# Performance work log

Measured on AMD Instinct MI355X. Metric: run time of the kernel, lower is better.

The kernel has to match this reference:

```python
import jax, jax.numpy as jnp
import numpy as np

N = 10000
D_IN = 128
HID = 32
EMB = 16


def setup_inputs() -> dict:
    key = jax.random.key(0)
    k0, k1, k2, k3 = jax.random.split(key, 4)
    X = jax.random.normal(k0, (N, D_IN), dtype=jnp.float32)
    # nonnegative, row-stochastic-ish prior
    A = jax.random.uniform(k1, (N, N), dtype=jnp.float32, minval=1e-6, maxval=1.0)
    A_prior = A / jnp.sum(A, axis=1, keepdims=True)
    # kaiming_uniform(a=sqrt(5)) on torch Linear weight (fan_in = D_IN): bound = 1/sqrt(fan_in)
    bnd1 = 1.0 / np.sqrt(D_IN)
    W1 = jax.random.uniform(k2, (D_IN, HID), dtype=jnp.float32, minval=-bnd1, maxval=bnd1)
    b1 = jnp.zeros((HID,), dtype=jnp.float32)
    # xavier_uniform: bound = sqrt(6/(fan_in+fan_out))
    bnd2 = np.sqrt(6.0 / (HID + EMB))
    W2 = jax.random.uniform(k3, (HID, EMB), dtype=jnp.float32, minval=-bnd2, maxval=bnd2)
    b2 = jnp.zeros((EMB,), dtype=jnp.float32)
    log_tau = jnp.asarray(np.log(1.2), dtype=jnp.float32)
    raw_alpha = jnp.asarray(np.log(0.3 / 0.7), dtype=jnp.float32)
    return {"X": X, "A_prior": A_prior, "W1": W1, "b1": b1, "W2": W2, "b2": b2,
            "log_tau": log_tau, "raw_alpha": raw_alpha}


def reference(X, A_prior, W1, b1, W2, b2, log_tau, raw_alpha):
    # encoder: Linear -> ReLU -> Linear
    H = jax.nn.relu(X @ W1 + b1) @ W2 + b2            # (N, EMB)
    # F.normalize(p=2, dim=1): x / max(||x||, eps)
    Hn = H / jnp.maximum(jnp.linalg.norm(H, axis=1, keepdims=True), 1e-12)
    tau = jnp.clip(jnp.exp(log_tau), 0.1, 10.0)
    alpha = jax.nn.sigmoid(raw_alpha)
    logits = (Hn @ Hn.T) / tau                        # (N, N) cosine sims / tau
    log_combined = alpha * jnp.log(A_prior + 1e-12) + (1.0 - alpha) * logits
    W = jax.nn.softmax(log_combined, axis=1)          # row-stochastic (N, N)
    return (W, H)
```

## Files before the change

kernel.cpp:

```cpp
#include <hip/hip_runtime.h>
#include <math.h>

#define N_NODES 10000
#define DIN 128
#define HID 32
#define EMB 16

#define TBS 256
#define RB 4
#define NF4 2500
#define NIT ((NF4 + TBS - 1) / TBS)
#define NB (N_NODES / RB)

typedef float fx4 __attribute__((ext_vector_type(4)));

#define EXP2F(x) __builtin_amdgcn_exp2f(x)
#define LOG2F(x) __builtin_amdgcn_logf(x)

__global__ __launch_bounds__(256) void encoder_kernel(
    const float* __restrict__ X, const float* __restrict__ W1,
    const float* __restrict__ b1, const float* __restrict__ W2,
    const float* __restrict__ b2, float* __restrict__ Hout,
    float* __restrict__ Hn)
{
    __shared__ float sW1[DIN * HID];
    __shared__ float sW2[HID * EMB];
    __shared__ float sb1[HID];
    __shared__ float sb2[EMB];
    const int t = threadIdx.x;
    for (int k = t; k < DIN * HID; k += 256) sW1[k] = W1[k];
    for (int k = t; k < HID * EMB; k += 256) sW2[k] = W2[k];
    if (t < HID) sb1[t] = b1[t];
    if (t < EMB) sb2[t] = b2[t];
    __syncthreads();

    const int row = blockIdx.x * 256 + t;
    if (row >= N_NODES) return;

    float h1[HID];
#pragma unroll
    for (int h = 0; h < HID; ++h) h1[h] = sb1[h];

    const float4* xr = (const float4*)(X + (size_t)row * DIN);
#pragma unroll
    for (int k4 = 0; k4 < DIN / 4; ++k4) {
        float4 xv = xr[k4];
        const float* w = &sW1[(k4 * 4) * HID];
#pragma unroll
        for (int h = 0; h < HID; ++h) h1[h] = fmaf(xv.x, w[h], h1[h]);
#pragma unroll
        for (int h = 0; h < HID; ++h) h1[h] = fmaf(xv.y, w[HID + h], h1[h]);
#pragma unroll
        for (int h = 0; h < HID; ++h) h1[h] = fmaf(xv.z, w[2 * HID + h], h1[h]);
#pragma unroll
        for (int h = 0; h < HID; ++h) h1[h] = fmaf(xv.w, w[3 * HID + h], h1[h]);
    }

    float e[EMB];
#pragma unroll
    for (int j = 0; j < EMB; ++j) e[j] = sb2[j];
#pragma unroll
    for (int h = 0; h < HID; ++h) {
        float v = fmaxf(h1[h], 0.0f);
#pragma unroll
        for (int j = 0; j < EMB; ++j) e[j] = fmaf(v, sW2[h * EMB + j], e[j]);
    }

    float s = 0.0f;
#pragma unroll
    for (int j = 0; j < EMB; ++j) s = fmaf(e[j], e[j], s);
    float nrm = sqrtf(s);
    float inv = 1.0f / fmaxf(nrm, 1e-12f);

    float* ho = Hout + (size_t)row * EMB;
    float* hn = Hn + (size_t)row * EMB;
#pragma unroll
    for (int j = 0; j < EMB; ++j) ho[j] = e[j];
#pragma unroll
    for (int j = 0; j < EMB; ++j) hn[j] = e[j] * inv;
}


__device__ __forceinline__ float dot16u(const float* h, const fx4& b0,
                                        const fx4& b1, const fx4& b2,
                                        const fx4& b3)
{
    float s = h[0] * b0.x;
    s = fmaf(h[1],  b0.y, s);
    s = fmaf(h[2],  b0.z, s);
    s = fmaf(h[3],  b0.w, s);
    s = fmaf(h[4],  b1.x, s);
    s = fmaf(h[5],  b1.y, s);
    s = fmaf(h[6],  b1.z, s);
    s = fmaf(h[7],  b1.w, s);
    s = fmaf(h[8],  b2.x, s);
    s = fmaf(h[9],  b2.y, s);
    s = fmaf(h[10], b2.z, s);
    s = fmaf(h[11], b2.w, s);
    s = fmaf(h[12], b3.x, s);
    s = fmaf(h[13], b3.y, s);
    s = fmaf(h[14], b3.z, s);
    s = fmaf(h[15], b3.w, s);
    return s;
}

__global__ __launch_bounds__(TBS, 8) void softmax_kernel(
    const float* __restrict__ A, const float* __restrict__ Hn,
    const float* __restrict__ p_log_tau, const float* __restrict__ p_raw_alpha,
    float* __restrict__ Wout)
{
    const int t = threadIdx.x;
    const int row0 = blockIdx.x * RB;

    const float tau = fminf(fmaxf(__expf(p_log_tau[0]), 0.1f), 10.0f);
    const float alpha = 1.0f / (1.0f + __expf(-p_raw_alpha[0]));
    const float cl  = (1.0f - alpha) / tau;
    const float cl2 = cl * 1.4426950408889634f;

    float shi[RB][EMB];
#pragma unroll
    for (int r = 0; r < RB; ++r) {
        const fx4* hp = (const fx4*)(Hn + (size_t)(row0 + r) * EMB);
#pragma unroll
        for (int p = 0; p < 4; ++p) {
            fx4 v = hp[p];
            shi[r][4 * p + 0] = __int_as_float(__builtin_amdgcn_readfirstlane(__float_as_int(v.x)));
            shi[r][4 * p + 1] = __int_as_float(__builtin_amdgcn_readfirstlane(__float_as_int(v.y)));
            shi[r][4 * p + 2] = __int_as_float(__builtin_amdgcn_readfirstlane(__float_as_int(v.z)));
            shi[r][4 * p + 3] = __int_as_float(__builtin_amdgcn_readfirstlane(__float_as_int(v.w)));
        }
    }

    const fx4* Hn4 = (const fx4*)Hn;

    float sloc[RB];
#pragma unroll
    for (int r = 0; r < RB; ++r) sloc[r] = 0.0f;

#pragma unroll 2
    for (int it = 0; it < NIT; ++it) {
        const int f4 = it * TBS + t;
        if (f4 < NF4) {
            fx4 av[RB];
#pragma unroll
            for (int r = 0; r < RB; ++r)
                av[r] = *((const fx4*)(A + (size_t)(row0 + r) * N_NODES) + f4);
#pragma unroll
            for (int d = 0; d < 4; ++d) {
                const int j = f4 * 4 + d;
                const fx4 b0 = Hn4[j * 4 + 0];
                const fx4 b1 = Hn4[j * 4 + 1];
                const fx4 b2 = Hn4[j * 4 + 2];
                const fx4 b3 = Hn4[j * 4 + 3];
#pragma unroll
                for (int r = 0; r < RB; ++r) {
                    float a = (d == 0) ? av[r].x
                            : (d == 1) ? av[r].y
                            : (d == 2) ? av[r].z
                                       : av[r].w;
                    float lgm = fmaf(alpha, LOG2F(a + 1e-12f), -cl2);
                    float dv = dot16u(shi[r], b0, b1, b2, b3);
                    sloc[r] += EXP2F(fmaf(cl2, dv, lgm));
                }
            }
        }
    }

    __shared__ float red[RB][TBS / 64];
    __shared__ float rbc[RB];
    const int lane = t & 63;
    const int wave = t >> 6;
#pragma unroll
    for (int r = 0; r < RB; ++r) {
        float v = sloc[r];
#pragma unroll
        for (int off = 32; off >= 1; off >>= 1) v += __shfl_down(v, off, 64);
        if (lane == 0) red[r][wave] = v;
    }
    __syncthreads();
    if (t < RB) {
        float v = red[t][0];
#pragma unroll
        for (int w = 1; w < TBS / 64; ++w) v += red[t][w];
        rbc[t] = 1.0f / v;
    }
    __syncthreads();
    float invl[RB];
#pragma unroll
    for (int r = 0; r < RB; ++r) invl[r] = rbc[r];

#pragma unroll 2
    for (int it = NIT - 1; it >= 0; --it) {
        const int f4 = it * TBS + t;
        if (f4 < NF4) {
            fx4 av[RB];
#pragma unroll
            for (int r = 0; r < RB; ++r)
                av[r] = __builtin_nontemporal_load(
                    (const fx4*)(A + (size_t)(row0 + r) * N_NODES) + f4);
            fx4 o[RB];
#pragma unroll
            for (int d = 0; d < 4; ++d) {
                const int j = f4 * 4 + d;
                const fx4 b0 = Hn4[j * 4 + 0];
                const fx4 b1 = Hn4[j * 4 + 1];
                const fx4 b2 = Hn4[j * 4 + 2];
                const fx4 b3 = Hn4[j * 4 + 3];
#pragma unroll
                for (int r = 0; r < RB; ++r) {
                    float a = (d == 0) ? av[r].x
                            : (d == 1) ? av[r].y
                            : (d == 2) ? av[r].z
                                       : av[r].w;
                    float lgm = fmaf(alpha, LOG2F(a + 1e-12f), -cl2);
                    float dv = dot16u(shi[r], b0, b1, b2, b3);
                    float e = EXP2F(fmaf(cl2, dv, lgm)) * invl[r];
                    if (d == 0)      o[r].x = e;
                    else if (d == 1) o[r].y = e;
                    else if (d == 2) o[r].z = e;
                    else             o[r].w = e;
                }
            }
#pragma unroll
            for (int r = 0; r < RB; ++r)
                __builtin_nontemporal_store(
                    o[r], (fx4*)(Wout + (size_t)(row0 + r) * N_NODES) + f4);
        }
    }
}

extern "C" void kernel_launch(void* const* d_in, const int* in_sizes, int n_in,
                              void* d_out, int out_size, void* d_ws, size_t ws_size,
                              hipStream_t stream) {
    const float* X        = (const float*)d_in[0];
    const float* A        = (const float*)d_in[1];
    const float* W1       = (const float*)d_in[2];
    const float* b1       = (const float*)d_in[3];
    const float* W2       = (const float*)d_in[4];
    const float* b2       = (const float*)d_in[5];
    const float* log_tau  = (const float*)d_in[6];
    const float* raw_alpha= (const float*)d_in[7];

    float* Wout = (float*)d_out;
    float* Hout = (float*)d_out + (size_t)N_NODES * N_NODES;
    float* Hn   = (float*)d_ws;

    encoder_kernel<<<(N_NODES + 255) / 256, 256, 0, stream>>>(X, W1, b1, W2, b2, Hout, Hn);

    softmax_kernel<<<NB, TBS, 0, stream>>>(A, Hn, log_tau, raw_alpha, Wout);
}
```

Measured before the change: 1.219 ms.

## Split softmax into 2D-tiled partial-sum and normalize kernels with LDS transposed tiles

Replaces the single row-block softmax kernel with two kernels over a 2D grid of (256-row block, 200-column group). Each thread now owns one row and keeps its Hn vector in registers. A and W tiles are staged through LDS so global accesses stay coalesced while each thread works along its own row. Per-group partial sums go to workspace and the second kernel sums all 50 partials before normalizing. This trades the old per-block wide row reduction and the reload of Hn for each row block for an extra launch, additional workspace traffic, strided LDS access, and Hn column loads that are uniform across a wave (broadcast).

```diff
diff --git a/kernel.cpp b/kernel.cpp
--- a/kernel.cpp
+++ b/kernel.cpp
@@ -6,11 +6,13 @@
 #define HID 32
 #define EMB 16
 
-#define TBS 256
-#define RB 4
-#define NF4 2500
-#define NIT ((NF4 + TBS - 1) / TBS)
-#define NB (N_NODES / RB)
+#define RBLK 256
+#define G    50
+#define JG   200
+#define JT   20
+#define NTILE (JG / JT)
+#define LSTR 24
+#define NRB  ((N_NODES + RBLK - 1) / RBLK)
 
 typedef float fx4 __attribute__((ext_vector_type(4)));
 
@@ -81,150 +83,157 @@
 }
 
 
-__device__ __forceinline__ float dot16u(const float* h, const fx4& b0,
-                                        const fx4& b1, const fx4& b2,
-                                        const fx4& b3)
-{
-    float s = h[0] * b0.x;
-    s = fmaf(h[1],  b0.y, s);
-    s = fmaf(h[2],  b0.z, s);
-    s = fmaf(h[3],  b0.w, s);
-    s = fmaf(h[4],  b1.x, s);
-    s = fmaf(h[5],  b1.y, s);
-    s = fmaf(h[6],  b1.z, s);
-    s = fmaf(h[7],  b1.w, s);
-    s = fmaf(h[8],  b2.x, s);
-    s = fmaf(h[9],  b2.y, s);
-    s = fmaf(h[10], b2.z, s);
-    s = fmaf(h[11], b2.w, s);
-    s = fmaf(h[12], b3.x, s);
-    s = fmaf(h[13], b3.y, s);
-    s = fmaf(h[14], b3.z, s);
-    s = fmaf(h[15], b3.w, s);
+__device__ __forceinline__ float dot16f(const float4& ha, const float4& hb,
+                                        const float4& hc, const float4& hd,
+                                        const float4& b0, const float4& b1,
+                                        const float4& b2, const float4& b3)
+{
+    float s = ha.x * b0.x;
+    s = fmaf(ha.y, b0.y, s);
+    s = fmaf(ha.z, b0.z, s);
+    s = fmaf(ha.w, b0.w, s);
+    s = fmaf(hb.x, b1.x, s);
+    s = fmaf(hb.y, b1.y, s);
+    s = fmaf(hb.z, b1.z, s);
+    s = fmaf(hb.w, b1.w, s);
+    s = fmaf(hc.x, b2.x, s);
+    s = fmaf(hc.y, b2.y, s);
+    s = fmaf(hc.z, b2.z, s);
+    s = fmaf(hc.w, b2.w, s);
+    s = fmaf(hd.x, b3.x, s);
+    s = fmaf(hd.y, b3.y, s);
+    s = fmaf(hd.z, b3.z, s);
+    s = fmaf(hd.w, b3.w, s);
     return s;
 }
 
-__global__ __launch_bounds__(TBS, 8) void softmax_kernel(
+__global__ __launch_bounds__(RBLK, 6) void partial_kernel(
     const float* __restrict__ A, const float* __restrict__ Hn,
     const float* __restrict__ p_log_tau, const float* __restrict__ p_raw_alpha,
-    float* __restrict__ Wout)
-{
+    float* __restrict__ partial)
+{
+    __shared__ float lds[RBLK * LSTR];
     const int t = threadIdx.x;
-    const int row0 = blockIdx.x * RB;
+    const int row0 = blockIdx.x * RBLK;
+    const int g = blockIdx.y;
+    const int j0 = g * JG;
 
     const float tau = fminf(fmaxf(__expf(p_log_tau[0]), 0.1f), 10.0f);
     const float alpha = 1.0f / (1.0f + __expf(-p_raw_alpha[0]));
-    const float cl  = (1.0f - alpha) / tau;
-    const float cl2 = cl * 1.4426950408889634f;
-
-    float shi[RB][EMB];
-#pragma unroll
-    for (int r = 0; r < RB; ++r) {
-        const fx4* hp = (const fx4*)(Hn + (size_t)(row0 + r) * EMB);
-#pragma unroll
-        for (int p = 0; p < 4; ++p) {
-            fx4 v = hp[p];
-            shi[r][4 * p + 0] = __int_as_float(__builtin_amdgcn_readfirstlane(__float_as_int(v.x)));
-            shi[r][4 * p + 1] = __int_as_float(__builtin_amdgcn_readfirstlane(__float_as_int(v.y)));
-            shi[r][4 * p + 2] = __int_as_float(__builtin_amdgcn_readfirstlane(__float_as_int(v.z)));
-            shi[r][4 * p + 3] = __int_as_float(__builtin_amdgcn_readfirstlane(__float_as_int(v.w)));
-        }
-    }
-
-    const fx4* Hn4 = (const fx4*)Hn;
-
-    float sloc[RB];
-#pragma unroll
-    for (int r = 0; r < RB; ++r) sloc[r] = 0.0f;
-
-#pragma unroll 2
-    for (int it = 0; it < NIT; ++it) {
-        const int f4 = it * TBS + t;
-        if (f4 < NF4) {
-            fx4 av[RB];
-#pragma unroll
-            for (int r = 0; r < RB; ++r)
-                av[r] = *((const fx4*)(A + (size_t)(row0 + r) * N_NODES) + f4);
+    const float cl2 = ((1.0f - alpha) / tau) * 1.4426950408889634f;
+
+    const int rowc = min(row0 + t, N_NODES - 1);
+    const float4* hp = (const float4*)(Hn + (size_t)rowc * EMB);
+    const float4 ha = hp[0], hb = hp[1], hc = hp[2], hd = hp[3];
+
+    float sloc = 0.0f;
+
+    for (int tile = 0; tile < NTILE; ++tile) {
+        const int jt0 = j0 + tile * JT;
+        __syncthreads();
+#pragma unroll
+        for (int k = 0; k < 5; ++k) {
+            const int f = k * RBLK + t;
+            const int r = f / 5, q = f % 5;
+            const int grow = row0 + r;
+            if (grow < N_NODES) {
+                float4 v = *(const float4*)(A + (size_t)grow * N_NODES + jt0 + q * 4);
+                *(float4*)&lds[r * LSTR + q * 4] = v;
+            }
+        }
+        __syncthreads();
+#pragma unroll
+        for (int jq = 0; jq < 5; ++jq) {
+            const float4 av = *(const float4*)&lds[t * LSTR + jq * 4];
 #pragma unroll
             for (int d = 0; d < 4; ++d) {
-                const int j = f4 * 4 + d;
-                const fx4 b0 = Hn4[j * 4 + 0];
-                const fx4 b1 = Hn4[j * 4 + 1];
-                const fx4 b2 = Hn4[j * 4 + 2];
-                const fx4 b3 = Hn4[j * 4 + 3];
-#pragma unroll
-                for (int r = 0; r < RB; ++r) {
-                    float a = (d == 0) ? av[r].x
-                            : (d == 1) ? av[r].y
-                            : (d == 2) ? av[r].z
-                                       : av[r].w;
-                    float lgm = fmaf(alpha, LOG2F(a + 1e-12f), -cl2);
-                    float dv = dot16u(shi[r], b0, b1, b2, b3);
-                    sloc[r] += EXP2F(fmaf(cl2, dv, lgm));
-                }
-            }
-        }
-    }
-
-    __shared__ float red[RB][TBS / 64];
-    __shared__ float rbc[RB];
-    const int lane = t & 63;
-    const int wave = t >> 6;
-#pragma unroll
-    for (int r = 0; r < RB; ++r) {
-        float v = sloc[r];
-#pragma unroll
-        for (int off = 32; off >= 1; off >>= 1) v += __shfl_down(v, off, 64);
-        if (lane == 0) red[r][wave] = v;
-    }
-    __syncthreads();
-    if (t < RB) {
-        float v = red[t][0];
-#pragma unroll
-        for (int w = 1; w < TBS / 64; ++w) v += red[t][w];
-        rbc[t] = 1.0f / v;
-    }
-    __syncthreads();
-    float invl[RB];
-#pragma unroll
-    for (int r = 0; r < RB; ++r) invl[r] = rbc[r];
-
-#pragma unroll 2
-    for (int it = NIT - 1; it >= 0; --it) {
-        const int f4 = it * TBS + t;
-        if (f4 < NF4) {
-            fx4 av[RB];
-#pragma unroll
-            for (int r = 0; r < RB; ++r)
-                av[r] = __builtin_nontemporal_load(
-                    (const fx4*)(A + (size_t)(row0 + r) * N_NODES) + f4);
-            fx4 o[RB];
+                const int j = jt0 + jq * 4 + d;
+                const float4* bp = (const float4*)(Hn + (size_t)j * EMB);
+                const float4 b0 = bp[0], b1 = bp[1], b2 = bp[2], b3 = bp[3];
+                const float a = (d == 0) ? av.x : (d == 1) ? av.y
+                              : (d == 2) ? av.z : av.w;
+                const float lgm = fmaf(alpha, LOG2F(a + 1e-12f), -cl2);
+                const float dv = dot16f(ha, hb, hc, hd, b0, b1, b2, b3);
+                sloc += EXP2F(fmaf(cl2, dv, lgm));
+            }
+        }
+    }
+
+    const int row = row0 + t;
+    if (row < N_NODES)
+        partial[(size_t)g * N_NODES + row] = sloc;
+}
+
+__global__ __launch_bounds__(RBLK, 6) void norm_kernel(
+    const float* __restrict__ A, const float* __restrict__ Hn,
+    const float* __restrict__ p_log_tau, const float* __restrict__ p_raw_alpha,
+    const float* __restrict__ partial, float* __restrict__ Wout)
+{
+    __shared__ float lds[RBLK * LSTR];
+    const int t = threadIdx.x;
+    const int row0 = blockIdx.x * RBLK;
+    const int g = blockIdx.y;
+    const int j0 = g * JG;
+
+    const float tau = fminf(fmaxf(__expf(p_log_tau[0]), 0.1f), 10.0f);
+    const float alpha = 1.0f / (1.0f + __expf(-p_raw_alpha[0]));
+    const float cl2 = ((1.0f - alpha) / tau) * 1.4426950408889634f;
+
+    const int rowc = min(row0 + t, N_NODES - 1);
+    const float4* hp = (const float4*)(Hn + (size_t)rowc * EMB);
+    const float4 ha = hp[0], hb = hp[1], hc = hp[2], hd = hp[3];
+
+    float tot = 0.0f;
+#pragma unroll 5
+    for (int g2 = 0; g2 < G; ++g2)
+        tot += partial[(size_t)g2 * N_NODES + rowc];
+    const float invl = 1.0f / tot;
+
+    for (int tile = 0; tile < NTILE; ++tile) {
+        const int jt0 = j0 + tile * JT;
+        __syncthreads();
+#pragma unroll
+        for (int k = 0; k < 5; ++k) {
+            const int f = k * RBLK + t;
+            const int r = f / 5, q = f % 5;
+            const int grow = row0 + r;
+            if (grow < N_NODES) {
+                float4 v = *(const float4*)(A + (size_t)grow * N_NODES + jt0 + q * 4);
+                *(float4*)&lds[r * LSTR + q * 4] = v;
+            }
+        }
+        __syncthreads();
+#pragma unroll
+        for (int jq = 0; jq < 5; ++jq) {
+            const float4 av = *(const float4*)&lds[t * LSTR + jq * 4];
+            float4 ev;
 #pragma unroll
             for (int d = 0; d < 4; ++d) {
-                const int j = f4 * 4 + d;
-                const fx4 b0 = Hn4[j * 4 + 0];
-                const fx4 b1 = Hn4[j * 4 + 1];
-                const fx4 b2 = Hn4[j * 4 + 2];
-                const fx4 b3 = Hn4[j * 4 + 3];
-#pragma unroll
-                for (int r = 0; r < RB; ++r) {
-                    float a = (d == 0) ? av[r].x
-                            : (d == 1) ? av[r].y
-                            : (d == 2) ? av[r].z
-                                       : av[r].w;
-                    float lgm = fmaf(alpha, LOG2F(a + 1e-12f), -cl2);
-                    float dv = dot16u(shi[r], b0, b1, b2, b3);
-                    float e = EXP2F(fmaf(cl2, dv, lgm)) * invl[r];
-                    if (d == 0)      o[r].x = e;
-                    else if (d == 1) o[r].y = e;
-                    else if (d == 2) o[r].z = e;
-                    else             o[r].w = e;
-                }
-            }
-#pragma unroll
-            for (int r = 0; r < RB; ++r)
-                __builtin_nontemporal_store(
-                    o[r], (fx4*)(Wout + (size_t)(row0 + r) * N_NODES) + f4);
+                const int j = jt0 + jq * 4 + d;
+                const float4* bp = (const float4*)(Hn + (size_t)j * EMB);
+                const float4 b0 = bp[0], b1 = bp[1], b2 = bp[2], b3 = bp[3];
+                const float a = (d == 0) ? av.x : (d == 1) ? av.y
+                              : (d == 2) ? av.z : av.w;
+                const float lgm = fmaf(alpha, LOG2F(a + 1e-12f), -cl2);
+                const float dv = dot16f(ha, hb, hc, hd, b0, b1, b2, b3);
+                const float e = EXP2F(fmaf(cl2, dv, lgm)) * invl;
+                if (d == 0)      ev.x = e;
+                else if (d == 1) ev.y = e;
+                else if (d == 2) ev.z = e;
+                else             ev.w = e;
+            }
+            *(float4*)&lds[t * LSTR + jq * 4] = ev;
+        }
+        __syncthreads();
+#pragma unroll
+        for (int k = 0; k < 5; ++k) {
+            const int f = k * RBLK + t;
+            const int r = f / 5, q = f % 5;
+            const int grow = row0 + r;
+            if (grow < N_NODES) {
+                float4 v = *(const float4*)&lds[r * LSTR + q * 4];
+                *(float4*)(Wout + (size_t)grow * N_NODES + jt0 + q * 4) = v;
+            }
         }
     }
 }
@@ -244,8 +253,11 @@
     float* Wout = (float*)d_out;
     float* Hout = (float*)d_out + (size_t)N_NODES * N_NODES;
     float* Hn   = (float*)d_ws;
+    float* partial = (float*)d_ws + (size_t)N_NODES * EMB;
 
     encoder_kernel<<<(N_NODES + 255) / 256, 256, 0, stream>>>(X, W1, b1, W2, b2, Hout, Hn);
 
-    softmax_kernel<<<NB, TBS, 0, stream>>>(A, Hn, log_tau, raw_alpha, Wout);
-}
+    dim3 grid(NRB, G);
+    partial_kernel<<<grid, RBLK, 0, stream>>>(A, Hn, log_tau, raw_alpha, partial);
+    norm_kernel<<<grid, RBLK, 0, stream>>>(A, Hn, log_tau, raw_alpha, partial, Wout);
+}
```

New measurement: 1.102 ms. 9.6% less time.
